# Performance work log

Measured on AMD Instinct MI355X. Metric: run time of the kernel, lower is better.

Reference implementation:

```python
import jax, jax.numpy as jnp
import numpy as np

N = 50000
E = 800000


def gcn_conv(x, row, col, dinv_sqrt, W, b, n_nodes):
    # PyG GCNConv: x' = lin(x); out[col] += norm * x'[row]; out += bias
    # norm = dinv_sqrt[row] * dinv_sqrt[col] (self-loops already in row/col)
    xw = x @ W                                  # [N, out_dim]
    norm = dinv_sqrt[row] * dinv_sqrt[col]      # [E']
    msg = xw[row] * norm[:, None]               # [E', out_dim]
    out = jax.ops.segment_sum(msg, col, num_segments=n_nodes)
    return out + b


def setup_inputs() -> dict:
    key = jax.random.key(0)
    k1, k2, k3, k4 = jax.random.split(key, 4)
    x = jax.random.normal(k1, (N, 128), dtype=jnp.float32)
    edge_index = jax.random.randint(k2, (2, E), 0, N, dtype=jnp.int64)
    W1 = jax.random.normal(k3, (128, 64), dtype=jnp.float32) * (1.0 / np.sqrt(128))
    b1 = jnp.zeros((64,), dtype=jnp.float32)
    W2 = jax.random.normal(k4, (64, 32), dtype=jnp.float32) * (1.0 / np.sqrt(64))
    b2 = jnp.zeros((32,), dtype=jnp.float32)
    return {"x": x, "edge_index": edge_index, "W1": W1, "b1": b1, "W2": W2, "b2": b2}


def reference(x, edge_index, W1, b1, W2, b2):
    n_nodes = x.shape[0]
    # add self loops (fixed size -> jit friendly)
    loops = jnp.arange(n_nodes, dtype=edge_index.dtype)
    row = jnp.concatenate([edge_index[0], loops])  # source
    col = jnp.concatenate([edge_index[1], loops])  # target
    # symmetric normalization from in-degree (all edge weights = 1)
    deg = jax.ops.segment_sum(jnp.ones_like(col, dtype=x.dtype), col, num_segments=n_nodes)
    dinv_sqrt = jnp.where(deg > 0, jax.lax.rsqrt(deg), 0.0)

    h = gcn_conv(x, row, col, dinv_sqrt, W1, b1, n_nodes)
    h = jax.nn.relu(h)
    h = gcn_conv(h, row, col, dinv_sqrt, W2, b2, n_nodes)
    return jax.nn.log_softmax(h, axis=1)
```

## Files before the change

### kernel.cpp

```cpp
#include <hip/hip_runtime.h>

#define F0 128
#define F1 64
#define F2 32
#define CPB 256
#define EPB 4096

typedef unsigned short ushort_t;
typedef unsigned int uint_t;

__device__ __forceinline__ ushort_t f2bf(float f) {
    uint_t u = __float_as_uint(f);
    return (ushort_t)((u + 0x7FFFu + ((u >> 16) & 1u)) >> 16);
}
__device__ __forceinline__ float bflo(uint_t v) { return __uint_as_float(v << 16); }
__device__ __forceinline__ float bfhi(uint_t v) { return __uint_as_float(v & 0xFFFF0000u); }
__device__ __forceinline__ uint_t pack2(float a, float b) {
    return (uint_t)f2bf(a) | ((uint_t)f2bf(b) << 16);
}

__global__ __launch_bounds__(256) void bucket_count(const int* __restrict__ col,
                                                    int* __restrict__ bcnt_chunks, int E) {
    __shared__ int h[256];
    int t = threadIdx.x;
    h[t] = 0;
    __syncthreads();
    int e0 = blockIdx.x * EPB;
    int cnt = E - e0; if (cnt > EPB) cnt = EPB;
    for (int k = t; k < cnt; k += 256) atomicAdd(&h[col[e0 + k] >> 8], 1);
    __syncthreads();
    bcnt_chunks[blockIdx.x * 256 + t] = h[t];
}

__global__ __launch_bounds__(256) void per_bucket_scan(int* __restrict__ bcnt_chunks,
                                                       int nbC, int* __restrict__ btot) {
    __shared__ int s[256];
    int b = blockIdx.x;
    int t = threadIdx.x;
    int v = (t < nbC) ? bcnt_chunks[t * 256 + b] : 0;
    s[t] = v;
    __syncthreads();
    for (int off = 1; off < 256; off <<= 1) {
        int u = (t >= off) ? s[t - off] : 0;
        __syncthreads();
        s[t] += u;
        __syncthreads();
    }
    if (t < nbC) bcnt_chunks[t * 256 + b] = s[t] - v;
    if (t == 255) btot[b] = s[255];
}

__global__ __launch_bounds__(256) void bucket_base_scan(const int* __restrict__ btot,
                                                        int* __restrict__ bucket_base) {
    __shared__ int s[256];
    int t = threadIdx.x;
    int v = btot[t];
    s[t] = v;
    __syncthreads();
    for (int off = 1; off < 256; off <<= 1) {
        int u = (t >= off) ? s[t - off] : 0;
        __syncthreads();
        s[t] += u;
        __syncthreads();
    }
    bucket_base[t] = s[t] - v;
}

__global__ __launch_bounds__(256) void coarse_part(const int* __restrict__ row,
                                                   const int* __restrict__ col,
                                                   const int* __restrict__ run_local,
                                                   const int* __restrict__ bucket_base,
                                                   uint_t* __restrict__ ebuf, int E) {
    __shared__ uint_t stage[EPB];
    __shared__ int hist[256];
    __shared__ int hbase[256];
    int t = threadIdx.x;
    int e0 = blockIdx.x * EPB;
    int cnt = E - e0; if (cnt > EPB) cnt = EPB;
    hbase[t] = run_local[blockIdx.x * 256 + t] + bucket_base[t];
    hist[t] = 0;
    __syncthreads();
    for (int k = t; k < cnt; k += 256) {
        int c = col[e0 + k], r = row[e0 + k];
        stage[k] = ((uint_t)r << 16) | (uint_t)c;
    }
    __syncthreads();
    for (int k = t; k < cnt; k += 256) {
        uint_t p = stage[k];
        int b = (int)((p & 0xFFFFu) >> 8);
        int rk = atomicAdd(&hist[b], 1);
        ebuf[hbase[b] + rk] = p;
    }
}

__global__ __launch_bounds__(256) void fine_build(const int* __restrict__ bucket_base,
                                                  const uint_t* __restrict__ ebuf,
                                                  int* __restrict__ ptr,
                                                  float* __restrict__ dinv,
                                                  ushort_t* __restrict__ erow,
                                                  int N, int E, int nbuck) {
    __shared__ int hist[CPB];
    __shared__ int pref[CPB];
    int b = blockIdx.x;
    int cbase = b << 8;
    int t = threadIdx.x;
    int seg0 = bucket_base[b];
    int seg1 = (b + 1 < nbuck) ? bucket_base[b + 1] : E;
    hist[t] = 0;
    __syncthreads();
    for (int k = seg0 + t; k < seg1; k += 256)
        atomicAdd(&hist[ebuf[k] & 255u], 1);
    __syncthreads();
    int deg = hist[t];
    pref[t] = deg;
    __syncthreads();
    for (int off = 1; off < 256; off <<= 1) {
        int u = (t >= off) ? pref[t - off] : 0;
        __syncthreads();
        pref[t] += u;
        __syncthreads();
    }
    int base = seg0 + pref[t] - deg;
    int c = cbase + t;
    if (c < N) {
        ptr[c] = base;
        dinv[c] = rsqrtf((float)(deg + 1));
    }
    if (b == nbuck - 1 && t == 0) ptr[N] = E;
    __syncthreads();
    pref[t] = base;
    __syncthreads();
    for (int k = seg0 + t; k < seg1; k += 256) {
        uint_t p = ebuf[k];
        int pos = atomicAdd(&pref[p & 255u], 1);
        erow[pos] = (ushort_t)(p >> 16);
    }
}

__device__ __forceinline__ void fma4(float4& a, float xs, const float4& wv) {
    a.x = fmaf(xs, wv.x, a.x);
    a.y = fmaf(xs, wv.y, a.y);
    a.z = fmaf(xs, wv.z, a.z);
    a.w = fmaf(xs, wv.w, a.w);
}

__global__ __launch_bounds__(256) void gemm1(const float* __restrict__ x,
                                             const float* __restrict__ W,
                                             const float* __restrict__ dinv,
                                             ushort_t* __restrict__ xwb, int N) {
    __shared__ float Xl[64 * F0];
    __shared__ float Wl[F0 * F1];
    int tid = threadIdx.x;
    int base = blockIdx.x * 64;

    const float4* W4 = (const float4*)W;
    float4* Wl4 = (float4*)Wl;
#pragma unroll
    for (int i = 0; i < 8; ++i) Wl4[tid + 256 * i] = W4[tid + 256 * i];

    float4* Xl4 = (float4*)Xl;
#pragma unroll
    for (int i = 0; i < 8; ++i) {
        int idx = tid + 256 * i;
        int r = idx >> 5, c4 = idx & 31;
        int gr = base + r;
        float4 v = (gr < N) ? ((const float4*)x)[(size_t)gr * 32 + c4]
                            : make_float4(0.f, 0.f, 0.f, 0.f);
        Xl4[r * 32 + (c4 ^ (r >> 2))] = v;
    }
    __syncthreads();

    int tc = tid & 15, tr = tid >> 4;
    float4 acc0 = make_float4(0.f, 0.f, 0.f, 0.f);
    float4 acc1 = acc0, acc2 = acc0, acc3 = acc0;
    const float4* Wl4c = (const float4*)Wl;
    const float4* Xl4c = (const float4*)Xl;

#pragma unroll 4
    for (int kk = 0; kk < 32; ++kk) {
        float4 xv0 = Xl4c[(4 * tr + 0) * 32 + (kk ^ tr)];
        float4 xv1 = Xl4c[(4 * tr + 1) * 32 + (kk ^ tr)];
        float4 xv2 = Xl4c[(4 * tr + 2) * 32 + (kk ^ tr)];
        float4 xv3 = Xl4c[(4 * tr + 3) * 32 + (kk ^ tr)];
        float4 w0 = Wl4c[(4 * kk + 0) * 16 + tc];
        float4 w1 = Wl4c[(4 * kk + 1) * 16 + tc];
        float4 w2 = Wl4c[(4 * kk + 2) * 16 + tc];
        float4 w3 = Wl4c[(4 * kk + 3) * 16 + tc];
        fma4(acc0, xv0.x, w0); fma4(acc0, xv0.y, w1); fma4(acc0, xv0.z, w2); fma4(acc0, xv0.w, w3);
        fma4(acc1, xv1.x, w0); fma4(acc1, xv1.y, w1); fma4(acc1, xv1.z, w2); fma4(acc1, xv1.w, w3);
        fma4(acc2, xv2.x, w0); fma4(acc2, xv2.y, w1); fma4(acc2, xv2.z, w2); fma4(acc2, xv2.w, w3);
        fma4(acc3, xv3.x, w0); fma4(acc3, xv3.y, w1); fma4(acc3, xv3.z, w2); fma4(acc3, xv3.w, w3);
    }

    int gr = base + 4 * tr;
#pragma unroll
    for (int k = 0; k < 4; ++k) {
        int r = gr + k;
        if (r < N) {
            float d = dinv[r];
            float4 a = (k == 0) ? acc0 : (k == 1) ? acc1 : (k == 2) ? acc2 : acc3;
            ushort4 o = make_ushort4(f2bf(a.x * d), f2bf(a.y * d), f2bf(a.z * d), f2bf(a.w * d));
            *(ushort4*)(&xwb[(size_t)r * F1 + 4 * tc]) = o;
        }
    }
}

__global__ void agg1(const int* __restrict__ ptr, const ushort_t* __restrict__ erow,
                     const ushort_t* __restrict__ xwb, const float* __restrict__ dinv,
                     const float* __restrict__ b, ushort_t* __restrict__ h1b, int N) {
    int t = blockIdx.x * 256 + threadIdx.x;
    int i = t >> 6;
    if (i >= N) return;
    int l = t & 63, h = l >> 5, l2 = l & 31;
    const uint_t* xwb2 = (const uint_t*)xwb;

    float a0 = 0.f, a1 = 0.f;
    int e = ptr[i], end = ptr[i + 1];
    for (; e + 7 < end; e += 8) {
        int r0 = erow[e + 0 + h], r1 = erow[e + 2 + h];
        int r2 = erow[e + 4 + h], r3 = erow[e + 6 + h];
        uint_t v0 = xwb2[(size_t)r0 * 32 + l2];
        uint_t v1 = xwb2[(size_t)r1 * 32 + l2];
        uint_t v2 = xwb2[(size_t)r2 * 32 + l2];
        uint_t v3 = xwb2[(size_t)r3 * 32 + l2];
        a0 += bflo(v0); a1 += bfhi(v0);
        a0 += bflo(v1); a1 += bfhi(v1);
        a0 += bflo(v2); a1 += bfhi(v2);
        a0 += bflo(v3); a1 += bfhi(v3);
    }
    for (; e + 1 < end; e += 2) {
        int r0 = erow[e + h];
        uint_t v0 = xwb2[(size_t)r0 * 32 + l2];
        a0 += bflo(v0); a1 += bfhi(v0);
    }
    if (e < end && h == 0) {
        uint_t v0 = xwb2[(size_t)erow[e] * 32 + l2];
        a0 += bflo(v0); a1 += bfhi(v0);
    }
    a0 += __shfl_down(a0, 32, 64);
    a1 += __shfl_down(a1, 32, 64);
    if (h == 0) {
        uint_t sv = xwb2[(size_t)i * 32 + l2];
        a0 += bflo(sv); a1 += bfhi(sv);
        float d = dinv[i];
        float2 bb = ((const float2*)b)[l2];
        a0 = fmaxf(a0 * d + bb.x, 0.f);
        a1 = fmaxf(a1 * d + bb.y, 0.f);
        ((uint_t*)h1b)[(size_t)i * 32 + l2] = pack2(a0, a1);
    }
}

__global__ __launch_bounds__(256) void gemm2(const ushort_t* __restrict__ h1b,
                                             const float* __restrict__ W,
                                             const float* __restrict__ dinv,
                                             ushort_t* __restrict__ hwb, int N) {
    __shared__ float Hl[128 * F1];
    __shared__ float Wl[F1 * F2];
    int tid = threadIdx.x;
    int base = blockIdx.x * 128;

    const float4* W4 = (const float4*)W;
    float4* Wl4 = (float4*)Wl;
#pragma unroll
    for (int i = 0; i < 2; ++i) Wl4[tid + 256 * i] = W4[tid + 256 * i];

    const uint4* H4 = (const uint4*)h1b;
    float4* Hl4 = (float4*)Hl;
#pragma unroll
    for (int it = 0; it < 4; ++it) {
        int g = tid + 256 * it;
        int r = g >> 3, c8 = g & 7;
        int gr = base + r;
        uint4 v = (gr < N) ? H4[(size_t)gr * 8 + c8] : make_uint4(0, 0, 0, 0);
        float4 a, b2;
        a.x = bflo(v.x); a.y = bfhi(v.x);
        a.z = bflo(v.y); a.w = bfhi(v.y);
        b2.x = bflo(v.z); b2.y = bfhi(v.z);
        b2.z = bflo(v.w); b2.w = bfhi(v.w);
        int sw = (r >> 2) & 15;
        Hl4[r * 16 + ((2 * c8 + 0) ^ sw)] = a;
        Hl4[r * 16 + ((2 * c8 + 1) ^ sw)] = b2;
    }
    __syncthreads();

    int tc = tid & 7, tr = tid >> 3;
    float4 acc0 = make_float4(0.f, 0.f, 0.f, 0.f);
    float4 acc1 = acc0, acc2 = acc0, acc3 = acc0;
    const float4* Wl4c = (const float4*)Wl;
    const float4* Hl4c = (const float4*)Hl;

#pragma unroll 4
    for (int kk = 0; kk < 16; ++kk) {
        int sw = kk ^ (tr & 15);
        float4 xv0 = Hl4c[(4 * tr + 0) * 16 + sw];
        float4 xv1 = Hl4c[(4 * tr + 1) * 16 + sw];
        float4 xv2 = Hl4c[(4 * tr + 2) * 16 + sw];
        float4 xv3 = Hl4c[(4 * tr + 3) * 16 + sw];
        float4 w0 = Wl4c[(4 * kk + 0) * 8 + tc];
        float4 w1 = Wl4c[(4 * kk + 1) * 8 + tc];
        float4 w2 = Wl4c[(4 * kk + 2) * 8 + tc];
        float4 w3 = Wl4c[(4 * kk + 3) * 8 + tc];
        fma4(acc0, xv0.x, w0); fma4(acc0, xv0.y, w1); fma4(acc0, xv0.z, w2); fma4(acc0, xv0.w, w3);
        fma4(acc1, xv1.x, w0); fma4(acc1, xv1.y, w1); fma4(acc1, xv1.z, w2); fma4(acc1, xv1.w, w3);
        fma4(acc2, xv2.x, w0); fma4(acc2, xv2.y, w1); fma4(acc2, xv2.z, w2); fma4(acc2, xv2.w, w3);
        fma4(acc3, xv3.x, w0); fma4(acc3, xv3.y, w1); fma4(acc3, xv3.z, w2); fma4(acc3, xv3.w, w3);
    }

    int gr = base + 4 * tr;
#pragma unroll
    for (int k = 0; k < 4; ++k) {
        int r = gr + k;
        if (r < N) {
            float d = dinv[r];
            float4 a = (k == 0) ? acc0 : (k == 1) ? acc1 : (k == 2) ? acc2 : acc3;
            ushort4 o = make_ushort4(f2bf(a.x * d), f2bf(a.y * d), f2bf(a.z * d), f2bf(a.w * d));
            *(ushort4*)(&hwb[(size_t)r * F2 + 4 * tc]) = o;
        }
    }
}

__global__ void agg2_lsm(const int* __restrict__ ptr, const ushort_t* __restrict__ erow,
                         const ushort_t* __restrict__ hwb, const float* __restrict__ dinv,
                         const float* __restrict__ b, float* __restrict__ out, int N) {
    int t = blockIdx.x * 256 + threadIdx.x;
    int i = t >> 5;
    if (i >= N) return;
    int g = t & 31, h = g >> 4, l2 = g & 15;
    const uint_t* hwb2 = (const uint_t*)hwb;

    float a0 = 0.f, a1 = 0.f;
    int e = ptr[i], end = ptr[i + 1];
    for (; e + 7 < end; e += 8) {
        int r0 = erow[e + 0 + h], r1 = erow[e + 2 + h];
        int r2 = erow[e + 4 + h], r3 = erow[e + 6 + h];
        uint_t v0 = hwb2[(size_t)r0 * 16 + l2];
        uint_t v1 = hwb2[(size_t)r1 * 16 + l2];
        uint_t v2 = hwb2[(size_t)r2 * 16 + l2];
        uint_t v3 = hwb2[(size_t)r3 * 16 + l2];
        a0 += bflo(v0); a1 += bfhi(v0);
        a0 += bflo(v1); a1 += bfhi(v1);
        a0 += bflo(v2); a1 += bfhi(v2);
        a0 += bflo(v3); a1 += bfhi(v3);
    }
    for (; e + 1 < end; e += 2) {
        int r0 = erow[e + h];
        uint_t v0 = hwb2[(size_t)r0 * 16 + l2];
        a0 += bflo(v0); a1 += bfhi(v0);
    }
    if (e < end && h == 0) {
        uint_t v0 = hwb2[(size_t)erow[e] * 16 + l2];
        a0 += bflo(v0); a1 += bfhi(v0);
    }
    a0 += __shfl_down(a0, 16, 32);
    a1 += __shfl_down(a1, 16, 32);

    uint_t sv = hwb2[(size_t)i * 16 + l2];
    a0 += bflo(sv); a1 += bfhi(sv);
    float d = dinv[i];
    float2 bb = ((const float2*)b)[l2];
    a0 = a0 * d + bb.x;
    a1 = a1 * d + bb.y;

    float m = fmaxf(a0, a1);
    for (int off = 8; off; off >>= 1) m = fmaxf(m, __shfl_xor(m, off, 16));
    float s = expf(a0 - m) + expf(a1 - m);
    for (int off = 8; off; off >>= 1) s += __shfl_xor(s, off, 16);
    float ls = logf(s);
    if (h == 0)
        ((float2*)out)[(size_t)i * 16 + l2] = make_float2(a0 - m - ls, a1 - m - ls);
}

extern "C" void kernel_launch(void* const* d_in, const int* in_sizes, int n_in,
                              void* d_out, int out_size, void* d_ws, size_t ws_size,
                              hipStream_t stream) {
    const float* x  = (const float*)d_in[0];
    const int*   ei = (const int*)d_in[1];
    const float* W1 = (const float*)d_in[2];
    const float* b1 = (const float*)d_in[3];
    const float* W2 = (const float*)d_in[4];
    const float* b2 = (const float*)d_in[5];

    int N = in_sizes[0] / F0;
    int E = in_sizes[1] / 2;
    const int* row = ei;
    const int* col = ei + E;

    int nbC   = (E + EPB - 1) / EPB;
    int nbuck = (N + CPB - 1) / CPB;

    size_t Np = ((size_t)N + 63) & ~(size_t)63;
    size_t Ep = ((size_t)E + 63) & ~(size_t)63;
    size_t Cp = (((size_t)nbC * 256) + 63) & ~(size_t)63;
    int*      bcnt_chunks = (int*)d_ws;
    int*      btot        = bcnt_chunks + Cp;
    int*      bucket_base = btot + 256;
    int*      ptr         = bucket_base + 256 + 64;
    float*    dinv        = (float*)(ptr + Np + 64);
    ushort_t* erow        = (ushort_t*)(dinv + Np);
    uint_t*   ebuf        = (uint_t*)(erow + Ep);
    ushort_t* xwb         = (ushort_t*)(ebuf + Ep);
    ushort_t* h1b         = xwb + Np * F1;
    ushort_t* hwb         = h1b + Np * F1;
    float*    out2        = (float*)d_out;

    bucket_count<<<nbC, 256, 0, stream>>>(col, bcnt_chunks, E);
    per_bucket_scan<<<256, 256, 0, stream>>>(bcnt_chunks, nbC, btot);
    bucket_base_scan<<<1, 256, 0, stream>>>(btot, bucket_base);
    coarse_part<<<nbC, 256, 0, stream>>>(row, col, bcnt_chunks, bucket_base, ebuf, E);
    fine_build<<<nbuck, 256, 0, stream>>>(bucket_base, ebuf, ptr, dinv, erow, N, E, nbuck);

    gemm1<<<(N + 63) / 64, 256, 0, stream>>>(x, W1, dinv, xwb, N);
    agg1<<<(int)(((size_t)N * 64 + 255) / 256), 256, 0, stream>>>(ptr, erow, xwb, dinv, b1, h1b, N);
    gemm2<<<(N + 127) / 128, 256, 0, stream>>>(h1b, W2, dinv, hwb, N);
    agg2_lsm<<<(int)(((size_t)N * 32 + 255) / 256), 256, 0, stream>>>(ptr, erow, hwb, dinv, b2, out2, N);
}
```

Baseline: 111.2 us.

## Fuse five CSR-build kernels into one cooperative kernel with grid syncs

Merges the bucket count, per-bucket scan, base scan, coarse partition and fine build into a single cooperative launch of 256 blocks, separated by grid-wide barriers. Each block recomputes the bucket-base scan locally instead of running a separate single-block kernel. The goal is to remove the launch gaps between four kernels. In exchange it relies on grid.sync cost and on all 256 blocks being co-resident, and it fixes both the grid size and the bucket count at 256.

After: 212.0 us. 1.91x slower.

```diff
diff --git a/kernel.cpp b/kernel.cpp
--- a/kernel.cpp
+++ b/kernel.cpp
@@ -1,4 +1,7 @@
 #include <hip/hip_runtime.h>
+#include <hip/hip_cooperative_groups.h>
+
+namespace cg = cooperative_groups;
 
 #define F0 128
 #define F1 64
@@ -19,121 +22,122 @@
     return (uint_t)f2bf(a) | ((uint_t)f2bf(b) << 16);
 }
 
-__global__ __launch_bounds__(256) void bucket_count(const int* __restrict__ col,
-                                                    int* __restrict__ bcnt_chunks, int E) {
-    __shared__ int h[256];
-    int t = threadIdx.x;
-    h[t] = 0;
-    __syncthreads();
-    int e0 = blockIdx.x * EPB;
-    int cnt = E - e0; if (cnt > EPB) cnt = EPB;
-    for (int k = t; k < cnt; k += 256) atomicAdd(&h[col[e0 + k] >> 8], 1);
-    __syncthreads();
-    bcnt_chunks[blockIdx.x * 256 + t] = h[t];
-}
-
-__global__ __launch_bounds__(256) void per_bucket_scan(int* __restrict__ bcnt_chunks,
-                                                       int nbC, int* __restrict__ btot) {
-    __shared__ int s[256];
+__global__ __launch_bounds__(256) void csr_build(const int* __restrict__ row,
+                                                 const int* __restrict__ col,
+                                                 int* __restrict__ bcnt_chunks,
+                                                 int* __restrict__ btot,
+                                                 int* __restrict__ ptr,
+                                                 float* __restrict__ dinv,
+                                                 ushort_t* __restrict__ erow,
+                                                 uint_t* __restrict__ ebuf,
+                                                 int N, int E, int nbC, int nbuck) {
+    cg::grid_group grid = cg::this_grid();
+    __shared__ uint_t stage[EPB];
+    __shared__ int h1[256];
+    __shared__ int h2[256];
+    __shared__ int h3[256];
+    __shared__ int seg_sh[2];
     int b = blockIdx.x;
     int t = threadIdx.x;
-    int v = (t < nbC) ? bcnt_chunks[t * 256 + b] : 0;
-    s[t] = v;
+
+    if (b < nbC) {
+        h1[t] = 0;
+        __syncthreads();
+        int e0 = b * EPB;
+        int cnt = E - e0; if (cnt > EPB) cnt = EPB;
+        for (int k = t; k < cnt; k += 256) atomicAdd(&h1[col[e0 + k] >> 8], 1);
+        __syncthreads();
+        bcnt_chunks[b * 256 + t] = h1[t];
+    }
+    grid.sync();
+
+    {
+        int v = (t < nbC) ? bcnt_chunks[t * 256 + b] : 0;
+        h3[t] = v;
+        __syncthreads();
+        for (int off = 1; off < 256; off <<= 1) {
+            int u = (t >= off) ? h3[t - off] : 0;
+            __syncthreads();
+            h3[t] += u;
+            __syncthreads();
+        }
+        if (t < nbC) bcnt_chunks[t * 256 + b] = h3[t] - v;
+        if (t == 255) btot[b] = h3[255];
+    }
+    grid.sync();
+
+    int excl;
+    {
+        int bv = btot[t];
+        h3[t] = bv;
+        __syncthreads();
+        for (int off = 1; off < 256; off <<= 1) {
+            int u = (t >= off) ? h3[t - off] : 0;
+            __syncthreads();
+            h3[t] += u;
+            __syncthreads();
+        }
+        excl = h3[t] - bv;
+    }
     __syncthreads();
-    for (int off = 1; off < 256; off <<= 1) {
-        int u = (t >= off) ? s[t - off] : 0;
-        __syncthreads();
-        s[t] += u;
-        __syncthreads();
-    }
-    if (t < nbC) bcnt_chunks[t * 256 + b] = s[t] - v;
-    if (t == 255) btot[b] = s[255];
-}
-
-__global__ __launch_bounds__(256) void bucket_base_scan(const int* __restrict__ btot,
-                                                        int* __restrict__ bucket_base) {
-    __shared__ int s[256];
-    int t = threadIdx.x;
-    int v = btot[t];
-    s[t] = v;
-    __syncthreads();
-    for (int off = 1; off < 256; off <<= 1) {
-        int u = (t >= off) ? s[t - off] : 0;
-        __syncthreads();
-        s[t] += u;
-        __syncthreads();
-    }
-    bucket_base[t] = s[t] - v;
-}
-
-__global__ __launch_bounds__(256) void coarse_part(const int* __restrict__ row,
-                                                   const int* __restrict__ col,
-                                                   const int* __restrict__ run_local,
-                                                   const int* __restrict__ bucket_base,
-                                                   uint_t* __restrict__ ebuf, int E) {
-    __shared__ uint_t stage[EPB];
-    __shared__ int hist[256];
-    __shared__ int hbase[256];
-    int t = threadIdx.x;
-    int e0 = blockIdx.x * EPB;
-    int cnt = E - e0; if (cnt > EPB) cnt = EPB;
-    hbase[t] = run_local[blockIdx.x * 256 + t] + bucket_base[t];
-    hist[t] = 0;
-    __syncthreads();
-    for (int k = t; k < cnt; k += 256) {
-        int c = col[e0 + k], r = row[e0 + k];
-        stage[k] = ((uint_t)r << 16) | (uint_t)c;
-    }
-    __syncthreads();
-    for (int k = t; k < cnt; k += 256) {
-        uint_t p = stage[k];
-        int b = (int)((p & 0xFFFFu) >> 8);
-        int rk = atomicAdd(&hist[b], 1);
-        ebuf[hbase[b] + rk] = p;
-    }
-}
-
-__global__ __launch_bounds__(256) void fine_build(const int* __restrict__ bucket_base,
-                                                  const uint_t* __restrict__ ebuf,
-                                                  int* __restrict__ ptr,
-                                                  float* __restrict__ dinv,
-                                                  ushort_t* __restrict__ erow,
-                                                  int N, int E, int nbuck) {
-    __shared__ int hist[CPB];
-    __shared__ int pref[CPB];
-    int b = blockIdx.x;
-    int cbase = b << 8;
-    int t = threadIdx.x;
-    int seg0 = bucket_base[b];
-    int seg1 = (b + 1 < nbuck) ? bucket_base[b + 1] : E;
-    hist[t] = 0;
-    __syncthreads();
-    for (int k = seg0 + t; k < seg1; k += 256)
-        atomicAdd(&hist[ebuf[k] & 255u], 1);
-    __syncthreads();
-    int deg = hist[t];
-    pref[t] = deg;
-    __syncthreads();
-    for (int off = 1; off < 256; off <<= 1) {
-        int u = (t >= off) ? pref[t - off] : 0;
-        __syncthreads();
-        pref[t] += u;
-        __syncthreads();
-    }
-    int base = seg0 + pref[t] - deg;
-    int c = cbase + t;
-    if (c < N) {
-        ptr[c] = base;
-        dinv[c] = rsqrtf((float)(deg + 1));
-    }
-    if (b == nbuck - 1 && t == 0) ptr[N] = E;
-    __syncthreads();
-    pref[t] = base;
-    __syncthreads();
-    for (int k = seg0 + t; k < seg1; k += 256) {
-        uint_t p = ebuf[k];
-        int pos = atomicAdd(&pref[p & 255u], 1);
-        erow[pos] = (ushort_t)(p >> 16);
+
+    if (b < nbC) {
+        h2[t] = bcnt_chunks[b * 256 + t] + excl;
+        h1[t] = 0;
+        __syncthreads();
+        int e0 = b * EPB;
+        int cnt = E - e0; if (cnt > EPB) cnt = EPB;
+        for (int k = t; k < cnt; k += 256) {
+            int c = col[e0 + k], r = row[e0 + k];
+            stage[k] = ((uint_t)r << 16) | (uint_t)c;
+        }
+        __syncthreads();
+        for (int k = t; k < cnt; k += 256) {
+            uint_t p = stage[k];
+            int bk = (int)((p & 0xFFFFu) >> 8);
+            int rk = atomicAdd(&h1[bk], 1);
+            ebuf[h2[bk] + rk] = p;
+        }
+    }
+    grid.sync();
+
+    {
+        if (t == b) seg_sh[0] = excl;
+        if (b < 255 && t == b + 1) seg_sh[1] = excl;
+        if (b == 255 && t == 0) seg_sh[1] = E;
+        h1[t] = 0;
+        __syncthreads();
+        int seg0 = seg_sh[0];
+        int seg1 = seg_sh[1];
+        int cbase = b << 8;
+
+        for (int k = seg0 + t; k < seg1; k += 256)
+            atomicAdd(&h1[ebuf[k] & 255u], 1);
+        __syncthreads();
+        int deg = h1[t];
+        h2[t] = deg;
+        __syncthreads();
+        for (int off = 1; off < 256; off <<= 1) {
+            int u = (t >= off) ? h2[t - off] : 0;
+            __syncthreads();
+            h2[t] += u;
+            __syncthreads();
+        }
+        int base = seg0 + h2[t] - deg;
+        int c = cbase + t;
+        if (c < N) {
+            ptr[c] = base;
+            dinv[c] = rsqrtf((float)(deg + 1));
+        }
+        if (b == nbuck - 1 && t == 0) ptr[N] = E;
+        __syncthreads();
+        h2[t] = base;
+        __syncthreads();
+        for (int k = seg0 + t; k < seg1; k += 256) {
+            uint_t p = ebuf[k];
+            int pos = atomicAdd(&h2[p & 255u], 1);
+            erow[pos] = (ushort_t)(p >> 16);
+        }
     }
 }
 
@@ -393,8 +397,7 @@
     size_t Cp = (((size_t)nbC * 256) + 63) & ~(size_t)63;
     int*      bcnt_chunks = (int*)d_ws;
     int*      btot        = bcnt_chunks + Cp;
-    int*      bucket_base = btot + 256;
-    int*      ptr         = bucket_base + 256 + 64;
+    int*      ptr         = btot + 256 + 64;
     float*    dinv        = (float*)(ptr + Np + 64);
     ushort_t* erow        = (ushort_t*)(dinv + Np);
     uint_t*   ebuf        = (uint_t*)(erow + Ep);
@@ -403,11 +406,10 @@
     ushort_t* hwb         = h1b + Np * F1;
     float*    out2        = (float*)d_out;
 
-    bucket_count<<<nbC, 256, 0, stream>>>(col, bcnt_chunks, E);
-    per_bucket_scan<<<256, 256, 0, stream>>>(bcnt_chunks, nbC, btot);
-    bucket_base_scan<<<1, 256, 0, stream>>>(btot, bucket_base);
-    coarse_part<<<nbC, 256, 0, stream>>>(row, col, bcnt_chunks, bucket_base, ebuf, E);
-    fine_build<<<nbuck, 256, 0, stream>>>(bucket_base, ebuf, ptr, dinv, erow, N, E, nbuck);
+    void* args[] = {(void*)&row, (void*)&col, (void*)&bcnt_chunks, (void*)&btot,
+                    (void*)&ptr, (void*)&dinv, (void*)&erow, (void*)&ebuf,
+                    (void*)&N, (void*)&E, (void*)&nbC, (void*)&nbuck};
+    hipLaunchCooperativeKernel((void*)csr_build, dim3(256), dim3(256), args, 0, stream);
 
     gemm1<<<(N + 63) / 64, 256, 0, stream>>>(x, W1, dinv, xwb, N);
     agg1<<<(int)(((size_t)N * 64 + 255) / 256), 256, 0, stream>>>(ptr, erow, xwb, dinv, b1, h1b, N);
```
